# Optimization experiments

Measured on AMD Instinct MI355X. Metric: run time of the kernel, lower is better.

Reference implementation:

```python
import jax, jax.numpy as jnp
import numpy as np

EMBED_DIM = 1024
NUM_HEADS = 16
HEAD_DIM = EMBED_DIM // NUM_HEADS
SCALING = HEAD_DIM ** (-0.5)


def setup_inputs() -> dict:
    key = jax.random.key(0)
    ks = jax.random.split(key, 12)
    B, L, D = 2, 2048, EMBED_DIM
    s = 0.02
    return {
        "hidden_states": jax.random.normal(ks[0], (B, L, D), jnp.float32),
        "position_embeddings": jax.random.normal(ks[1], (B, L, D), jnp.float32),
        "attention_mask": jnp.zeros((1, L, L), jnp.float32),
        "Wq": jax.random.normal(ks[2], (D, D), jnp.float32) * s,
        "bq": jnp.zeros((D,), jnp.float32),
        "Wk": jax.random.normal(ks[3], (D, D), jnp.float32) * s,
        "bk": jnp.zeros((D,), jnp.float32),
        "Wv": jax.random.normal(ks[4], (D, D), jnp.float32) * s,
        "bv": jnp.zeros((D,), jnp.float32),
        "Wo": jax.random.normal(ks[5], (D, D), jnp.float32) * s,
        "bo": jnp.zeros((D,), jnp.float32),
    }


def _split_heads(x):
    # (B, L, D) -> (B, H, L, Dh)
    B, L, D = x.shape
    return x.reshape(B, L, NUM_HEADS, HEAD_DIM).transpose(0, 2, 1, 3)


def reference(hidden_states, position_embeddings, attention_mask,
              Wq, bq, Wk, bk, Wv, bv, Wo, bo):
    B, L, D = hidden_states.shape
    h_pe = hidden_states + position_embeddings   # query/key input
    q = _split_heads((h_pe @ Wq.T + bq) * SCALING)        # (B,H,L,Dh)
    k = _split_heads(h_pe @ Wk.T + bk)                    # (B,H,L,Dh)
    v = _split_heads(hidden_states @ Wv.T + bv)           # value: NO pos embed
    scores = jnp.einsum('bhqd,bhkd->bhqk', q, k)          # (B,H,L,L)
    scores = scores + attention_mask[:, None, :, :]       # mask broadcasts over heads
    probs = jax.nn.softmax(scores, axis=-1)               # dropout p=0.0 -> identity
    attn = jnp.einsum('bhqk,bhkd->bhqd', probs, v)        # (B,H,L,Dh)
    attn = attn.transpose(0, 2, 1, 3).reshape(B, L, D)    # merge heads
    return attn @ Wo.T + bo
```

## Files before the change

kernel.cpp:

```cpp
#include <hip/hip_runtime.h>

typedef __bf16 bf16x8 __attribute__((ext_vector_type(8)));
typedef unsigned short u16x8 __attribute__((ext_vector_type(8)));
typedef float f32x4 __attribute__((ext_vector_type(4)));
typedef float f32x16 __attribute__((ext_vector_type(16)));

constexpr int B_ = 2, L_ = 2048, D_ = 1024, H_ = 16, Dh_ = 64;
constexpr float LOG2E = 1.44269504088896f;
constexpr float SCALE_Q = 0.125f * LOG2E;

#define WAIT0_BARRIER() do { asm volatile("s_waitcnt vmcnt(0)" ::: "memory"); \
  __builtin_amdgcn_s_barrier(); asm volatile("" ::: "memory"); } while (0)
#define PLAIN_BARRIER() do { asm volatile("" ::: "memory"); \
  __builtin_amdgcn_s_barrier(); asm volatile("" ::: "memory"); } while (0)

__device__ __forceinline__ unsigned short f2bf(float x) {
  __bf16 h = (__bf16)x;
  return __builtin_bit_cast(unsigned short, h);
}
__device__ __forceinline__ unsigned int cvtpk(float lo, float hi) {
  unsigned int r;
  asm("v_cvt_pk_bf16_f32 %0, %1, %2" : "=v"(r) : "v"(lo), "v"(hi));
  return r;
}
__device__ __forceinline__ float exp2r(float x) {
  float r;
  asm("v_exp_f32 %0, %1" : "=v"(r) : "v"(x));
  return r;
}
__device__ __forceinline__ void gload16(const void* g, void* l) {
  __builtin_amdgcn_global_load_lds(
      (const __attribute__((address_space(1))) unsigned int*)g,
      (__attribute__((address_space(3))) unsigned int*)l, 16, 0, 0);
}

__global__ __launch_bounds__(256) void k_pre(const float* __restrict__ hs,
                                             const float* __restrict__ pe,
                                             const float* __restrict__ Wq,
                                             const float* __restrict__ Wk,
                                             const float* __restrict__ Wv,
                                             const float* __restrict__ Wo,
                                             const float* __restrict__ mask,
                                             unsigned short* __restrict__ hpe,
                                             unsigned short* __restrict__ hid,
                                             unsigned short* __restrict__ wq,
                                             unsigned short* __restrict__ wk,
                                             unsigned short* __restrict__ wv,
                                             unsigned short* __restrict__ wo,
                                             unsigned char* __restrict__ mflag) {
  int b = blockIdx.x, t = threadIdx.x;
  if (b < 4096) {
    int i = b * 256 + t;
    float4 h = reinterpret_cast<const float4*>(hs)[i];
    float4 p = reinterpret_cast<const float4*>(pe)[i];
    ushort4 x, y;
    x.x = f2bf(h.x + p.x); x.y = f2bf(h.y + p.y); x.z = f2bf(h.z + p.z); x.w = f2bf(h.w + p.w);
    y.x = f2bf(h.x); y.y = f2bf(h.y); y.z = f2bf(h.z); y.w = f2bf(h.w);
    reinterpret_cast<ushort4*>(hpe)[i] = x;
    reinterpret_cast<ushort4*>(hid)[i] = y;
  } else if (b < 8192) {
    int bb = b - 4096;
    int wsel = bb >> 10;
    int i = (bb & 1023) * 256 + t;
    const float* src = wsel == 0 ? Wq : wsel == 1 ? Wk : wsel == 2 ? Wv : Wo;
    unsigned short* dst = wsel == 0 ? wq : wsel == 1 ? wk : wsel == 2 ? wv : wo;
    float4 v = reinterpret_cast<const float4*>(src)[i];
    ushort4 r;
    r.x = f2bf(v.x); r.y = f2bf(v.y); r.z = f2bf(v.z); r.w = f2bf(v.w);
    reinterpret_cast<ushort4*>(dst)[i] = r;
  } else {
    int rg = b - 8192;
    int qt = rg >> 5, kt = rg & 31;
    int row = qt * 32 + (t >> 3);
    int col = kt * 64 + (t & 7) * 8;
    const float* mp = mask + (long)row * L_ + col;
    float4 a = *reinterpret_cast<const float4*>(mp);
    float4 c = *reinterpret_cast<const float4*>(mp + 4);
    bool nz = (a.x != 0.f) | (a.y != 0.f) | (a.z != 0.f) | (a.w != 0.f) |
              (c.x != 0.f) | (c.y != 0.f) | (c.z != 0.f) | (c.w != 0.f);
    __shared__ unsigned int sf[4];
    unsigned long long wb = __ballot(nz);
    int wave = t >> 6, lane = t & 63;
    if (lane == 0) sf[wave] = (wb != 0ULL);
    __syncthreads();
    if (t == 0) mflag[rg] = (sf[0] | sf[1] | sf[2] | sf[3]) ? 1 : 0;
  }
}

struct QkvArgs {
  const unsigned short *A0, *A1, *A2, *W0, *W1, *W2;
  const float *b0, *b1, *b2;
  unsigned short *o0, *o1, *o2;
};

__global__ __launch_bounds__(256) void k_qkv(QkvArgs q) {
  constexpr int K = 1024;
  __shared__ __align__(16) unsigned short As[2][128 * 64];
  __shared__ __align__(16) unsigned short Ws[2][128 * 64];
  const int z = blockIdx.z;
  const unsigned short* A = z == 0 ? q.A0 : z == 1 ? q.A1 : q.A2;
  const unsigned short* W = z == 0 ? q.W0 : z == 1 ? q.W1 : q.W2;
  const float* bias = z == 0 ? q.b0 : z == 1 ? q.b1 : q.b2;
  unsigned short* out = z == 0 ? q.o0 : z == 1 ? q.o1 : q.o2;
  const float scale = z == 0 ? SCALE_Q : 1.0f;

  const int t = threadIdx.x;
  const int m0 = blockIdx.x * 128, n0 = blockIdx.y * 128;
  const int wave = t >> 6, lane = t & 63, lg = lane >> 4, lr = lane & 15;
  const int wr = wave >> 1, wc = wave & 1;
  int rr[4], pp[4];
#pragma unroll
  for (int j = 0; j < 4; ++j) {
    int c = j * 256 + t;
    rr[j] = c >> 3;
    pp[j] = (c & 7) ^ (rr[j] & 7);
  }

  f32x4 acc[4][4] = {};

#pragma unroll
  for (int j = 0; j < 4; ++j) {
    gload16(A + (m0 + rr[j]) * K + pp[j] * 8, (char*)As[0] + j * 4096 + wave * 1024);
    gload16(W + (n0 + rr[j]) * K + pp[j] * 8, (char*)Ws[0] + j * 4096 + wave * 1024);
  }

  for (int kt = 0; kt < K / 64; ++kt) {
    const int cur = kt & 1;
    WAIT0_BARRIER();
    if (kt < K / 64 - 1) {
      const int k0 = (kt + 1) * 64;
#pragma unroll
      for (int j = 0; j < 4; ++j) {
        gload16(A + (m0 + rr[j]) * K + k0 + pp[j] * 8, (char*)As[cur ^ 1] + j * 4096 + wave * 1024);
        gload16(W + (n0 + rr[j]) * K + k0 + pp[j] * 8, (char*)Ws[cur ^ 1] + j * 4096 + wave * 1024);
      }
    }
#pragma unroll
    for (int kk = 0; kk < 2; ++kk) {
      bf16x8 a[4], b[4];
#pragma unroll
      for (int i = 0; i < 4; ++i) {
        int ra = wr * 64 + i * 16 + lr;
        int rb = wc * 64 + i * 16 + lr;
        a[i] = *reinterpret_cast<const bf16x8*>(As[cur] + ra * 64 + (((kk * 4 + lg) ^ (ra & 7)) * 8));
        b[i] = *reinterpret_cast<const bf16x8*>(Ws[cur] + rb * 64 + (((kk * 4 + lg) ^ (rb & 7)) * 8));
      }
#pragma unroll
      for (int i = 0; i < 4; ++i)
#pragma unroll
        for (int j = 0; j < 4; ++j)
          acc[i][j] = __builtin_amdgcn_mfma_f32_16x16x32_bf16(a[i], b[j], acc[i][j], 0, 0, 0);
    }
  }

  if (z == 2) {
#pragma unroll
    for (int i = 0; i < 4; ++i) {
#pragma unroll
      for (int j = 0; j < 4; ++j) {
        int n = n0 + wc * 64 + j * 16 + lr;
        int l0 = m0 + wr * 64 + i * 16 + lg * 4;
        int bb = l0 >> 11, l = l0 & 2047, hh = n >> 6, dd = n & 63;
        float bn = bias[n];
        ushort4 pk;
        pk.x = f2bf(acc[i][j][0] + bn);
        pk.y = f2bf(acc[i][j][1] + bn);
        pk.z = f2bf(acc[i][j][2] + bn);
        pk.w = f2bf(acc[i][j][3] + bn);
        *reinterpret_cast<ushort4*>(out + (((long)(bb * H_ + hh) * Dh_ + dd) * L_ + l)) = pk;
      }
    }
  } else {
#pragma unroll
    for (int i = 0; i < 4; ++i) {
#pragma unroll
      for (int j = 0; j < 4; ++j) {
        int n = n0 + wc * 64 + j * 16 + lr;
#pragma unroll
        for (int r = 0; r < 4; ++r) {
          int m = m0 + wr * 64 + i * 16 + lg * 4 + r;
          float v = (acc[i][j][r] + bias[n]) * scale;
          int bb = m >> 11, ll = m & 2047, hh = n >> 6, dd = n & 63;
          out[(((long)(bb * H_ + hh) * L_) + ll) * Dh_ + dd] = f2bf(v);
        }
      }
    }
  }
}

__global__ __launch_bounds__(256) void k_outp(const unsigned short* __restrict__ A,
                                              const unsigned short* __restrict__ W,
                                              const float* __restrict__ bias,
                                              float* __restrict__ out) {
  constexpr int K = 1024;
  __shared__ __align__(16) unsigned short As[2][128 * 64];
  __shared__ __align__(16) unsigned short Ws[2][64 * 64];
  const int t = threadIdx.x;
  const int m0 = blockIdx.x * 128, n0 = blockIdx.y * 64;
  const int wave = t >> 6, lane = t & 63, lg = lane >> 4, lr = lane & 15;
  int rr[4], pp[4];
#pragma unroll
  for (int j = 0; j < 4; ++j) {
    int c = j * 256 + t;
    rr[j] = c >> 3;
    pp[j] = (c & 7) ^ (rr[j] & 7);
  }
  int wrr[2], wpp[2];
#pragma unroll
  for (int j = 0; j < 2; ++j) {
    int c = j * 256 + t;
    wrr[j] = c >> 3;
    wpp[j] = (c & 7) ^ (wrr[j] & 7);
  }

  f32x4 acc[2][4] = {};

#pragma unroll
  for (int j = 0; j < 4; ++j)
    gload16(A + (m0 + rr[j]) * K + pp[j] * 8, (char*)As[0] + j * 4096 + wave * 1024);
#pragma unroll
  for (int j = 0; j < 2; ++j)
    gload16(W + (n0 + wrr[j]) * K + wpp[j] * 8, (char*)Ws[0] + j * 4096 + wave * 1024);

  for (int kt = 0; kt < K / 64; ++kt) {
    const int cur = kt & 1;
    WAIT0_BARRIER();
    if (kt < K / 64 - 1) {
      const int k0 = (kt + 1) * 64;
#pragma unroll
      for (int j = 0; j < 4; ++j)
        gload16(A + (m0 + rr[j]) * K + k0 + pp[j] * 8, (char*)As[cur ^ 1] + j * 4096 + wave * 1024);
#pragma unroll
      for (int j = 0; j < 2; ++j)
        gload16(W + (n0 + wrr[j]) * K + k0 + wpp[j] * 8, (char*)Ws[cur ^ 1] + j * 4096 + wave * 1024);
    }
#pragma unroll
    for (int kk = 0; kk < 2; ++kk) {
      bf16x8 a[2], b[4];
#pragma unroll
      for (int i = 0; i < 2; ++i) {
        int ra = wave * 32 + i * 16 + lr;
        a[i] = *reinterpret_cast<const bf16x8*>(As[cur] + ra * 64 + (((kk * 4 + lg) ^ (ra & 7)) * 8));
      }
#pragma unroll
      for (int j = 0; j < 4; ++j) {
        int rb = j * 16 + lr;
        b[j] = *reinterpret_cast<const bf16x8*>(Ws[cur] + rb * 64 + (((kk * 4 + lg) ^ (rb & 7)) * 8));
      }
#pragma unroll
      for (int i = 0; i < 2; ++i)
#pragma unroll
        for (int j = 0; j < 4; ++j)
          acc[i][j] = __builtin_amdgcn_mfma_f32_16x16x32_bf16(a[i], b[j], acc[i][j], 0, 0, 0);
    }
  }

#pragma unroll
  for (int i = 0; i < 2; ++i) {
#pragma unroll
    for (int j = 0; j < 4; ++j) {
      int n = n0 + j * 16 + lr;
      float bn = bias[n];
#pragma unroll
      for (int r = 0; r < 4; ++r) {
        int m = m0 + wave * 32 + i * 16 + lg * 4 + r;
        out[(long)m * D_ + n] = acc[i][j][r] + bn;
      }
    }
  }
}

__global__ __launch_bounds__(512) void k_attn(const unsigned short* __restrict__ Q,
                                              const unsigned short* __restrict__ Kg,
                                              const unsigned short* __restrict__ Vtg,
                                              const float* __restrict__ mask,
                                              const unsigned char* __restrict__ mflag,
                                              unsigned short* __restrict__ attn) {
  __shared__ __align__(16) unsigned short Ks[2][2][64 * 64];
  __shared__ __align__(16) unsigned short Vs[2][2][64 * 64];
  const int t = threadIdx.x;
  const int bid = blockIdx.x;
  const int sw = (bid & 7) * 64 + (bid >> 3);
  const int bh = sw >> 4, qt = sw & 15;
  const int h = bh & 15, bb = bh >> 4;
  const int wave = t >> 6, lane = t & 63;
  const int g = wave >> 2, wq = wave & 3;
  const int ql = lane & 31, hi = lane >> 5;
  const int q0w = qt * 128 + wq * 32;

  const unsigned short* Qh = Q + (long)bh * L_ * Dh_;
  const unsigned short* Kh = Kg + (long)bh * L_ * Dh_;
  const unsigned short* Vh = Vtg + (long)bh * Dh_ * L_;

  bf16x8 bq[4];
#pragma unroll
  for (int c = 0; c < 4; ++c)
    bq[c] = *reinterpret_cast<const bf16x8*>(Qh + (q0w + ql) * Dh_ + c * 16 + hi * 8);

  unsigned char mb = mflag[(q0w >> 5) * 32 + ql];
  unsigned long long mbits = __ballot((lane < 32) && (mb != 0));

  float lr0 = 0.f, lr1 = 0.f;
  f32x16 accO0 = {}, accO1 = {};

  const int tg = t & 255;
  const int c0 = tg, c1 = 256 + tg;
  const int r0 = c0 >> 3, s0g = (c0 & 7) ^ (r0 & 7);
  const int r1 = c1 >> 3, s1g = (c1 & 7) ^ (r1 & 7);

  {
    const unsigned short* K0 = Kh + g * 16 * 64 * Dh_;
    const unsigned short* V0 = Vh + g * 16 * 64;
    gload16(K0 + r0 * Dh_ + s0g * 8, (char*)&Ks[g][0][0] + wq * 1024);
    gload16(K0 + r1 * Dh_ + s1g * 8, (char*)&Ks[g][0][0] + 4096 + wq * 1024);
    gload16(V0 + r0 * L_ + s0g * 8, (char*)&Vs[g][0][0] + wq * 1024);
    gload16(V0 + r1 * L_ + s1g * 8, (char*)&Vs[g][0][0] + 4096 + wq * 1024);
  }

  for (int kl = 0; kl < 16; ++kl) {
    const int kt = g * 16 + kl;
    const int cur = kl & 1;

    WAIT0_BARRIER();

    if (kl < 15) {
      const unsigned short* Kt = Kh + (kt + 1) * 64 * Dh_;
      const unsigned short* Vn = Vh + (kt + 1) * 64;
      gload16(Kt + r0 * Dh_ + s0g * 8, (char*)&Ks[g][cur ^ 1][0] + wq * 1024);
      gload16(Kt + r1 * Dh_ + s1g * 8, (char*)&Ks[g][cur ^ 1][0] + 4096 + wq * 1024);
      gload16(Vn + r0 * L_ + s0g * 8, (char*)&Vs[g][cur ^ 1][0] + wq * 1024);
      gload16(Vn + r1 * L_ + s1g * 8, (char*)&Vs[g][cur ^ 1][0] + 4096 + wq * 1024);
    }

    const unsigned short* Kb = &Ks[g][cur][0];
    f32x16 s0 = {}, s1 = {};
#pragma unroll
    for (int c = 0; c < 4; ++c) {
      int colsw = (c * 16 + hi * 8) ^ ((ql & 7) << 3);
      bf16x8 ak0 = *reinterpret_cast<const bf16x8*>(Kb + ql * 64 + colsw);
      bf16x8 ak1 = *reinterpret_cast<const bf16x8*>(Kb + (32 + ql) * 64 + colsw);
      s0 = __builtin_amdgcn_mfma_f32_32x32x16_bf16(ak0, bq[c], s0, 0, 0, 0);
      s1 = __builtin_amdgcn_mfma_f32_32x32x16_bf16(ak1, bq[c], s1, 0, 0, 0);
    }

    if ((mbits >> kt) & 1ULL) {
      const float* mrow = mask + (long)(q0w + ql) * L_;
#pragma unroll
      for (int rg = 0; rg < 4; ++rg) {
        float4 mv = *reinterpret_cast<const float4*>(mrow + kt * 64 + rg * 8 + hi * 4);
        s0[4 * rg + 0] = fmaf(mv.x, LOG2E, s0[4 * rg + 0]);
        s0[4 * rg + 1] = fmaf(mv.y, LOG2E, s0[4 * rg + 1]);
        s0[4 * rg + 2] = fmaf(mv.z, LOG2E, s0[4 * rg + 2]);
        s0[4 * rg + 3] = fmaf(mv.w, LOG2E, s0[4 * rg + 3]);
      }
#pragma unroll
      for (int rg = 0; rg < 4; ++rg) {
        float4 mv = *reinterpret_cast<const float4*>(mrow + kt * 64 + 32 + rg * 8 + hi * 4);
        s1[4 * rg + 0] = fmaf(mv.x, LOG2E, s1[4 * rg + 0]);
        s1[4 * rg + 1] = fmaf(mv.y, LOG2E, s1[4 * rg + 1]);
        s1[4 * rg + 2] = fmaf(mv.z, LOG2E, s1[4 * rg + 2]);
        s1[4 * rg + 3] = fmaf(mv.w, LOG2E, s1[4 * rg + 3]);
      }
    }

    unsigned int w[16];
#pragma unroll
    for (int a = 0; a < 4; ++a) {
      float p0 = exp2r(s0[4 * a + 0]);
      float p1 = exp2r(s0[4 * a + 1]);
      float p2 = exp2r(s0[4 * a + 2]);
      float p3 = exp2r(s0[4 * a + 3]);
      lr0 += (p0 + p1) + (p2 + p3);
      w[2 * a] = cvtpk(p0, p1);
      w[2 * a + 1] = cvtpk(p2, p3);
    }
#pragma unroll
    for (int a = 0; a < 4; ++a) {
      float p0 = exp2r(s1[4 * a + 0]);
      float p1 = exp2r(s1[4 * a + 1]);
      float p2 = exp2r(s1[4 * a + 2]);
      float p3 = exp2r(s1[4 * a + 3]);
      lr1 += (p0 + p1) + (p2 + p3);
      w[8 + 2 * a] = cvtpk(p0, p1);
      w[9 + 2 * a] = cvtpk(p2, p3);
    }

    const unsigned short* Vb = &Vs[g][cur][0];
#pragma unroll
    for (int kc = 0; kc < 4; ++kc) {
      unsigned int pre0 = hi ? w[4 * kc + 0] : w[4 * kc + 2];
      unsigned int pre1 = hi ? w[4 * kc + 1] : w[4 * kc + 3];
      unsigned int cr0 = __shfl_xor(pre0, 32);
      unsigned int cr1 = __shfl_xor(pre1, 32);
      uint4 bw;
      bw.x = hi ? cr0 : w[4 * kc + 0];
      bw.y = hi ? cr1 : w[4 * kc + 1];
      bw.z = hi ? w[4 * kc + 2] : cr0;
      bw.w = hi ? w[4 * kc + 3] : cr1;
      bf16x8 bp = __builtin_bit_cast(bf16x8, bw);
      int colsw = (kc * 16 + hi * 8) ^ ((ql & 7) << 3);
      bf16x8 av0 = *reinterpret_cast<const bf16x8*>(Vb + ql * 64 + colsw);
      bf16x8 av1 = *reinterpret_cast<const bf16x8*>(Vb + (32 + ql) * 64 + colsw);
      accO0 = __builtin_amdgcn_mfma_f32_32x32x16_bf16(av0, bp, accO0, 0, 0, 0);
      accO1 = __builtin_amdgcn_mfma_f32_32x32x16_bf16(av1, bp, accO1, 0, 0, 0);
    }
  }

  PLAIN_BARRIER();

  float lrun = lr0 + lr1;
  float* accsh = reinterpret_cast<float*>(&Ks[0][0][0]);
  float* lsh = reinterpret_cast<float*>(&Vs[0][0][0]);
  if (g == 1) {
#pragma unroll
    for (int r = 0; r < 16; ++r) {
      accsh[r * 256 + wq * 64 + lane] = accO0[r];
      accsh[(16 + r) * 256 + wq * 64 + lane] = accO1[r];
    }
    lsh[wq * 64 + lane] = lrun;
  }
  __syncthreads();
  if (g == 0) {
#pragma unroll
    for (int r = 0; r < 16; ++r) {
      accO0[r] += accsh[r * 256 + wq * 64 + lane];
      accO1[r] += accsh[(16 + r) * 256 + wq * 64 + lane];
    }
    lrun += lsh[wq * 64 + lane];
    lrun += __shfl_xor(lrun, 32);
    float inv = 1.0f / lrun;
    unsigned short* orow = attn + (long)(bb * L_ + q0w + ql) * D_ + h * Dh_;
#pragma unroll
    for (int rg = 0; rg < 4; ++rg) {
      ushort4 pk;
      pk.x = f2bf(accO0[4 * rg + 0] * inv);
      pk.y = f2bf(accO0[4 * rg + 1] * inv);
      pk.z = f2bf(accO0[4 * rg + 2] * inv);
      pk.w = f2bf(accO0[4 * rg + 3] * inv);
      *reinterpret_cast<ushort4*>(orow + rg * 8 + hi * 4) = pk;
    }
#pragma unroll
    for (int rg = 0; rg < 4; ++rg) {
      ushort4 pk;
      pk.x = f2bf(accO1[4 * rg + 0] * inv);
      pk.y = f2bf(accO1[4 * rg + 1] * inv);
      pk.z = f2bf(accO1[4 * rg + 2] * inv);
      pk.w = f2bf(accO1[4 * rg + 3] * inv);
      *reinterpret_cast<ushort4*>(orow + 32 + rg * 8 + hi * 4) = pk;
    }
  }
}

extern "C" void kernel_launch(void* const* d_in, const int* in_sizes, int n_in,
                              void* d_out, int out_size, void* d_ws, size_t ws_size,
                              hipStream_t stream) {
  const float* hs   = (const float*)d_in[0];
  const float* pe   = (const float*)d_in[1];
  const float* mask = (const float*)d_in[2];
  const float* Wq   = (const float*)d_in[3];
  const float* bq   = (const float*)d_in[4];
  const float* Wk   = (const float*)d_in[5];
  const float* bk   = (const float*)d_in[6];
  const float* Wv   = (const float*)d_in[7];
  const float* bv   = (const float*)d_in[8];
  const float* Wo   = (const float*)d_in[9];
  const float* bo   = (const float*)d_in[10];

  unsigned short* ws  = (unsigned short*)d_ws;
  unsigned short* hpe = ws;
  unsigned short* hid = hpe + 4096 * 1024;
  unsigned short* wqb = hid + 4096 * 1024;
  unsigned short* wkb = wqb + 1024 * 1024;
  unsigned short* wvb = wkb + 1024 * 1024;
  unsigned short* wob = wvb + 1024 * 1024;
  unsigned short* Qb  = wob + 1024 * 1024;
  unsigned short* Kb  = Qb + 4194304;
  unsigned short* Vb  = Kb + 4194304;
  unsigned short* Ab  = Vb + 4194304;
  unsigned char*  mfl = (unsigned char*)(Ab + 4194304);

  k_pre<<<10240, 256, 0, stream>>>(hs, pe, Wq, Wk, Wv, Wo, mask,
                                   hpe, hid, wqb, wkb, wvb, wob, mfl);

  QkvArgs qa{hpe, hpe, hid, wqb, wkb, wvb, bq, bk, bv, Qb, Kb, Vb};
  k_qkv<<<dim3(32, 8, 3), 256, 0, stream>>>(qa);

  k_attn<<<512, 512, 0, stream>>>(Qb, Kb, Vb, mask, mfl, Ab);

  k_outp<<<dim3(32, 16), 256, 0, stream>>>(Ab, wob, bo, (float*)d_out);
}
```

Measured before the change: 128.2 us.

## Give each attention wave private K/V tiles and drop block barriers

The attention kernel is restructured so that each wave streams its own 32-key K/V tiles into a private LDS region, with only per-wave vmcnt waits instead of block-wide barriers per tile. Blocks shrink to 256 threads covering 64 queries, and the grid doubles to 1024. V is loaded through registers and written into a padded LDS layout rather than through direct-to-LDS loads. The aim is to remove barrier stalls and raise occupancy. In exchange, K/V data is loaded redundantly per wave, which raises global/L2 traffic, and each step does smaller MFMA work.

Result: slower. 150.3 us (+17.2%).

```diff
diff --git a/kernel.cpp b/kernel.cpp
--- a/kernel.cpp
+++ b/kernel.cpp
@@ -13,6 +13,7 @@
   __builtin_amdgcn_s_barrier(); asm volatile("" ::: "memory"); } while (0)
 #define PLAIN_BARRIER() do { asm volatile("" ::: "memory"); \
   __builtin_amdgcn_s_barrier(); asm volatile("" ::: "memory"); } while (0)
+#define WAVE_WAIT0() asm volatile("s_waitcnt vmcnt(0)" ::: "memory")
 
 __device__ __forceinline__ unsigned short f2bf(float x) {
   __bf16 h = (__bf16)x;
@@ -270,27 +271,27 @@
   }
 }
 
-__global__ __launch_bounds__(512) void k_attn(const unsigned short* __restrict__ Q,
+__global__ __launch_bounds__(256) void k_attn(const unsigned short* __restrict__ Q,
                                               const unsigned short* __restrict__ Kg,
                                               const unsigned short* __restrict__ Vtg,
                                               const float* __restrict__ mask,
                                               const unsigned char* __restrict__ mflag,
                                               unsigned short* __restrict__ attn) {
-  __shared__ __align__(16) unsigned short Ks[2][2][64 * 64];
-  __shared__ __align__(16) unsigned short Vs[2][2][64 * 64];
+  __shared__ __align__(16) unsigned short KsW[4][2][32 * 64];
+  __shared__ __align__(16) unsigned short VsW[4][64 * 40];
   const int t = threadIdx.x;
   const int bid = blockIdx.x;
-  const int sw = (bid & 7) * 64 + (bid >> 3);
-  const int bh = sw >> 4, qt = sw & 15;
+  const int sw = (bid & 7) * 128 + (bid >> 3);
+  const int bh = sw >> 5, qt = sw & 31;
   const int h = bh & 15, bb = bh >> 4;
   const int wave = t >> 6, lane = t & 63;
-  const int g = wave >> 2, wq = wave & 3;
+  const int qsub = wave >> 1, g = wave & 1;
   const int ql = lane & 31, hi = lane >> 5;
-  const int q0w = qt * 128 + wq * 32;
+  const int q0w = qt * 64 + qsub * 32;
 
   const unsigned short* Qh = Q + (long)bh * L_ * Dh_;
-  const unsigned short* Kh = Kg + (long)bh * L_ * Dh_;
-  const unsigned short* Vh = Vtg + (long)bh * Dh_ * L_;
+  const unsigned short* Kh = Kg + (long)bh * L_ * Dh_ + (long)g * 1024 * Dh_;
+  const unsigned short* Vh = Vtg + (long)bh * Dh_ * L_ + g * 1024;
 
   bf16x8 bq[4];
 #pragma unroll
@@ -303,91 +304,75 @@
   float lr0 = 0.f, lr1 = 0.f;
   f32x16 accO0 = {}, accO1 = {};
 
-  const int tg = t & 255;
-  const int c0 = tg, c1 = 256 + tg;
-  const int r0 = c0 >> 3, s0g = (c0 & 7) ^ (r0 & 7);
-  const int r1 = c1 >> 3, s1g = (c1 & 7) ^ (r1 & 7);
-
-  {
-    const unsigned short* K0 = Kh + g * 16 * 64 * Dh_;
-    const unsigned short* V0 = Vh + g * 16 * 64;
-    gload16(K0 + r0 * Dh_ + s0g * 8, (char*)&Ks[g][0][0] + wq * 1024);
-    gload16(K0 + r1 * Dh_ + s1g * 8, (char*)&Ks[g][0][0] + 4096 + wq * 1024);
-    gload16(V0 + r0 * L_ + s0g * 8, (char*)&Vs[g][0][0] + wq * 1024);
-    gload16(V0 + r1 * L_ + s1g * 8, (char*)&Vs[g][0][0] + 4096 + wq * 1024);
-  }
-
-  for (int kl = 0; kl < 16; ++kl) {
-    const int kt = g * 16 + kl;
-    const int cur = kl & 1;
-
-    WAIT0_BARRIER();
-
-    if (kl < 15) {
-      const unsigned short* Kt = Kh + (kt + 1) * 64 * Dh_;
-      const unsigned short* Vn = Vh + (kt + 1) * 64;
-      gload16(Kt + r0 * Dh_ + s0g * 8, (char*)&Ks[g][cur ^ 1][0] + wq * 1024);
-      gload16(Kt + r1 * Dh_ + s1g * 8, (char*)&Ks[g][cur ^ 1][0] + 4096 + wq * 1024);
-      gload16(Vn + r0 * L_ + s0g * 8, (char*)&Vs[g][cur ^ 1][0] + wq * 1024);
-      gload16(Vn + r1 * L_ + s1g * 8, (char*)&Vs[g][cur ^ 1][0] + 4096 + wq * 1024);
-    }
-
-    const unsigned short* Kb = &Ks[g][cur][0];
-    f32x16 s0 = {}, s1 = {};
+  const int krow = lane >> 3;
+  const int kslot = (lane & 7) ^ krow;
+  const int vrow = lane >> 2;
+  const int vslot = lane & 3;
+
+  unsigned short* Vw = &VsW[wave][0];
+  u16x8 vreg[4];
+
+#pragma unroll
+  for (int j = 0; j < 4; ++j)
+    gload16(Kh + (j * 8 + krow) * Dh_ + kslot * 8, (char*)&KsW[wave][0][0] + j * 1024);
+#pragma unroll
+  for (int j = 0; j < 4; ++j)
+    vreg[j] = *reinterpret_cast<const u16x8*>(Vh + (j * 16 + vrow) * L_ + vslot * 8);
+
+  for (int kt2 = 0; kt2 < 32; ++kt2) {
+    const int cur = kt2 & 1;
+
+    WAVE_WAIT0();
+
+#pragma unroll
+    for (int j = 0; j < 4; ++j)
+      *reinterpret_cast<u16x8*>(Vw + (j * 16 + vrow) * 40 + vslot * 8) = vreg[j];
+
+    if (kt2 < 31) {
+      const unsigned short* Kt = Kh + (kt2 + 1) * 32 * Dh_;
+      const unsigned short* Vn = Vh + (kt2 + 1) * 32;
+#pragma unroll
+      for (int j = 0; j < 4; ++j)
+        gload16(Kt + (j * 8 + krow) * Dh_ + kslot * 8, (char*)&KsW[wave][cur ^ 1][0] + j * 1024);
+#pragma unroll
+      for (int j = 0; j < 4; ++j)
+        vreg[j] = *reinterpret_cast<const u16x8*>(Vn + (j * 16 + vrow) * L_ + vslot * 8);
+    }
+
+    const unsigned short* Kb = &KsW[wave][cur][0];
+    f32x16 s0 = {};
 #pragma unroll
     for (int c = 0; c < 4; ++c) {
-      int colsw = (c * 16 + hi * 8) ^ ((ql & 7) << 3);
-      bf16x8 ak0 = *reinterpret_cast<const bf16x8*>(Kb + ql * 64 + colsw);
-      bf16x8 ak1 = *reinterpret_cast<const bf16x8*>(Kb + (32 + ql) * 64 + colsw);
-      s0 = __builtin_amdgcn_mfma_f32_32x32x16_bf16(ak0, bq[c], s0, 0, 0, 0);
-      s1 = __builtin_amdgcn_mfma_f32_32x32x16_bf16(ak1, bq[c], s1, 0, 0, 0);
-    }
-
-    if ((mbits >> kt) & 1ULL) {
-      const float* mrow = mask + (long)(q0w + ql) * L_;
+      bf16x8 ak = *reinterpret_cast<const bf16x8*>(Kb + ql * 64 + (((2 * c + hi) ^ (ql & 7)) * 8));
+      s0 = __builtin_amdgcn_mfma_f32_32x32x16_bf16(ak, bq[c], s0, 0, 0, 0);
+    }
+
+    if ((mbits >> (g * 16 + (kt2 >> 1))) & 1ULL) {
+      const float* mrow = mask + (long)(q0w + ql) * L_ + g * 1024 + kt2 * 32;
 #pragma unroll
       for (int rg = 0; rg < 4; ++rg) {
-        float4 mv = *reinterpret_cast<const float4*>(mrow + kt * 64 + rg * 8 + hi * 4);
+        float4 mv = *reinterpret_cast<const float4*>(mrow + rg * 8 + hi * 4);
         s0[4 * rg + 0] = fmaf(mv.x, LOG2E, s0[4 * rg + 0]);
         s0[4 * rg + 1] = fmaf(mv.y, LOG2E, s0[4 * rg + 1]);
         s0[4 * rg + 2] = fmaf(mv.z, LOG2E, s0[4 * rg + 2]);
         s0[4 * rg + 3] = fmaf(mv.w, LOG2E, s0[4 * rg + 3]);
       }
-#pragma unroll
-      for (int rg = 0; rg < 4; ++rg) {
-        float4 mv = *reinterpret_cast<const float4*>(mrow + kt * 64 + 32 + rg * 8 + hi * 4);
-        s1[4 * rg + 0] = fmaf(mv.x, LOG2E, s1[4 * rg + 0]);
-        s1[4 * rg + 1] = fmaf(mv.y, LOG2E, s1[4 * rg + 1]);
-        s1[4 * rg + 2] = fmaf(mv.z, LOG2E, s1[4 * rg + 2]);
-        s1[4 * rg + 3] = fmaf(mv.w, LOG2E, s1[4 * rg + 3]);
-      }
-    }
-
-    unsigned int w[16];
+    }
+
+    unsigned int w[8];
 #pragma unroll
     for (int a = 0; a < 4; ++a) {
       float p0 = exp2r(s0[4 * a + 0]);
       float p1 = exp2r(s0[4 * a + 1]);
       float p2 = exp2r(s0[4 * a + 2]);
       float p3 = exp2r(s0[4 * a + 3]);
-      lr0 += (p0 + p1) + (p2 + p3);
+      if (a & 1) lr1 += (p0 + p1) + (p2 + p3); else lr0 += (p0 + p1) + (p2 + p3);
       w[2 * a] = cvtpk(p0, p1);
       w[2 * a + 1] = cvtpk(p2, p3);
     }
-#pragma unroll
-    for (int a = 0; a < 4; ++a) {
-      float p0 = exp2r(s1[4 * a + 0]);
-      float p1 = exp2r(s1[4 * a + 1]);
-      float p2 = exp2r(s1[4 * a + 2]);
-      float p3 = exp2r(s1[4 * a + 3]);
-      lr1 += (p0 + p1) + (p2 + p3);
-      w[8 + 2 * a] = cvtpk(p0, p1);
-      w[9 + 2 * a] = cvtpk(p2, p3);
-    }
-
-    const unsigned short* Vb = &Vs[g][cur][0];
-#pragma unroll
-    for (int kc = 0; kc < 4; ++kc) {
+
+#pragma unroll
+    for (int kc = 0; kc < 2; ++kc) {
       unsigned int pre0 = hi ? w[4 * kc + 0] : w[4 * kc + 2];
       unsigned int pre1 = hi ? w[4 * kc + 1] : w[4 * kc + 3];
       unsigned int cr0 = __shfl_xor(pre0, 32);
@@ -398,36 +383,35 @@
       bw.z = hi ? w[4 * kc + 2] : cr0;
       bw.w = hi ? w[4 * kc + 3] : cr1;
       bf16x8 bp = __builtin_bit_cast(bf16x8, bw);
-      int colsw = (kc * 16 + hi * 8) ^ ((ql & 7) << 3);
-      bf16x8 av0 = *reinterpret_cast<const bf16x8*>(Vb + ql * 64 + colsw);
-      bf16x8 av1 = *reinterpret_cast<const bf16x8*>(Vb + (32 + ql) * 64 + colsw);
+      bf16x8 av0 = *reinterpret_cast<const bf16x8*>(Vw + ql * 40 + (kc * 2 + hi) * 8);
+      bf16x8 av1 = *reinterpret_cast<const bf16x8*>(Vw + (32 + ql) * 40 + (kc * 2 + hi) * 8);
       accO0 = __builtin_amdgcn_mfma_f32_32x32x16_bf16(av0, bp, accO0, 0, 0, 0);
       accO1 = __builtin_amdgcn_mfma_f32_32x32x16_bf16(av1, bp, accO1, 0, 0, 0);
     }
   }
 
-  PLAIN_BARRIER();
-
   float lrun = lr0 + lr1;
-  float* accsh = reinterpret_cast<float*>(&Ks[0][0][0]);
-  float* lsh = reinterpret_cast<float*>(&Vs[0][0][0]);
+  lrun += __shfl_xor(lrun, 32);
+
+  __syncthreads();
+  float* accsh = reinterpret_cast<float*>(&KsW[0][0][0]);
+  float* lsh = reinterpret_cast<float*>(&VsW[0][0]);
   if (g == 1) {
 #pragma unroll
     for (int r = 0; r < 16; ++r) {
-      accsh[r * 256 + wq * 64 + lane] = accO0[r];
-      accsh[(16 + r) * 256 + wq * 64 + lane] = accO1[r];
-    }
-    lsh[wq * 64 + lane] = lrun;
+      accsh[(qsub * 32 + r) * 64 + lane] = accO0[r];
+      accsh[(qsub * 32 + 16 + r) * 64 + lane] = accO1[r];
+    }
+    lsh[qsub * 64 + lane] = lrun;
   }
   __syncthreads();
   if (g == 0) {
 #pragma unroll
     for (int r = 0; r < 16; ++r) {
-      accO0[r] += accsh[r * 256 + wq * 64 + lane];
-      accO1[r] += accsh[(16 + r) * 256 + wq * 64 + lane];
-    }
-    lrun += lsh[wq * 64 + lane];
-    lrun += __shfl_xor(lrun, 32);
+      accO0[r] += accsh[(qsub * 32 + r) * 64 + lane];
+      accO1[r] += accsh[(qsub * 32 + 16 + r) * 64 + lane];
+    }
+    lrun += lsh[qsub * 64 + lane];
     float inv = 1.0f / lrun;
     unsigned short* orow = attn + (long)(bb * L_ + q0w + ql) * D_ + h * Dh_;
 #pragma unroll
@@ -485,7 +469,7 @@
   QkvArgs qa{hpe, hpe, hid, wqb, wkb, wvb, bq, bk, bv, Qb, Kb, Vb};
   k_qkv<<<dim3(32, 8, 3), 256, 0, stream>>>(qa);
 
-  k_attn<<<512, 512, 0, stream>>>(Qb, Kb, Vb, mask, mfl, Ab);
+  k_attn<<<1024, 256, 0, stream>>>(Qb, Kb, Vb, mask, mfl, Ab);
 
   k_outp<<<dim3(32, 16), 256, 0, stream>>>(Ab, wob, bo, (float*)d_out);
 }
```
